# Optimization experiments

Hardware: AMD Instinct MI355X
Metric: run time of the kernel (lower is better)

Reference implementation:

```python
import jax, jax.numpy as jnp
import numpy as np

N = 100000          # num nodes
E_C = 6_400_000     # connection edges
E_D = 400_000       # destination edges
F_IN = 5
H = 8
BN_EPS = 1e-5
L2_EPS = 1e-12


def setup_inputs() -> dict:
    key = jax.random.key(0)
    ks = jax.random.split(key, 16)
    d = {}
    d["x"] = jax.random.normal(ks[0], (N, F_IN), dtype=jnp.float32)
    d["edge_index_connections"] = jax.random.randint(ks[1], (2, E_C), 0, N, dtype=jnp.int64)
    d["edge_index_destinations"] = jax.random.randint(ks[2], (2, E_D), 0, N, dtype=jnp.int64)
    # SAGEConv weights: lin_l (neighbor aggregate), lin_r (root), no bias
    d["W1l"] = jax.random.normal(ks[3], (H, F_IN), jnp.float32) * 0.3
    d["W1r"] = jax.random.normal(ks[4], (H, F_IN), jnp.float32) * 0.3
    d["W2l"] = jax.random.normal(ks[5], (H, H), jnp.float32) * 0.3
    d["W2r"] = jax.random.normal(ks[6], (H, H), jnp.float32) * 0.3
    d["W3l"] = jax.random.normal(ks[7], (H, H), jnp.float32) * 0.3
    d["W3r"] = jax.random.normal(ks[8], (H, H), jnp.float32) * 0.3
    d["W4l"] = jax.random.normal(ks[9], (H, H), jnp.float32) * 0.3
    d["W4r"] = jax.random.normal(ks[10], (H, H), jnp.float32) * 0.3
    # LazyBatchNorm1d affine params (init gamma=1, beta=0)
    for i in range(1, 5):
        d[f"g{i}"] = jnp.ones((H,), jnp.float32)
        d[f"b{i}"] = jnp.zeros((H,), jnp.float32)
    return d


def _sage(x, ei, Wl, Wr):
    # PyG SAGEConv(mean aggr, normalize=True, bias=False):
    # out = lin_l(mean_{j in N(i)} x_j) + lin_r(x_i); then L2 normalize rows.
    src, dst = ei[0], ei[1]
    msgs = x[src]                                            # [E, F] gather
    s = jax.ops.segment_sum(msgs, dst, num_segments=N)       # [N, F]
    cnt = jax.ops.segment_sum(jnp.ones((ei.shape[1],), x.dtype), dst, num_segments=N)
    mean = s / jnp.maximum(cnt, 1.0)[:, None]                # zero for isolated nodes
    out = mean @ Wl.T + x @ Wr.T                             # [N, H]
    nrm = jnp.linalg.norm(out, axis=-1, keepdims=True)
    return out / jnp.maximum(nrm, L2_EPS)


def _bn(x, g, b):
    # BatchNorm1d in training mode: per-feature batch stats (biased variance)
    m = x.mean(axis=0)
    v = x.var(axis=0)
    return (x - m) * jax.lax.rsqrt(v + BN_EPS) * g + b


def reference(x, edge_index_connections, edge_index_destinations,
              W1l, W1r, W2l, W2r, W3l, W3r, W4l, W4r,
              g1, b1, g2, b2, g3, b3, g4, b4):
    eic = edge_index_connections
    eid = edge_index_destinations
    h = _bn(jax.nn.relu(_sage(x, eic, W1l, W1r)), g1, b1)
    # ITERATIONS_BEFORE_DESTINATION = 1 (conv4 + bn2)
    h = _bn(jax.nn.relu(_sage(h, eic, W4l, W4r)), g2, b2)
    # destination pass (conv2 + bn3)
    h = _bn(jax.nn.relu(_sage(h, eid, W2l, W2r)), g3, b3)
    # ITERATIONS_AFTER_DESTINATION = 2 (conv3 + bn4)
    for _ in range(2):
        h = _bn(jax.nn.relu(_sage(h, eic, W3l, W3r)), g4, b4)
    return h
```

## Files before the change

### kernel.cpp

```cpp
#include <hip/hip_runtime.h>
#include <hip/hip_fp16.h>

#define NN 100000
#define EC 6400000
#define ED 400000
#define BN_EPS 1e-5f
#define NB 391
#define CAPC 18432
#define CAPD 2048
#define EPB 8192
#define NBK_C 782
#define NBK_D 49
#define PREPB 16


__global__ __launch_bounds__(1024)
void zero_small(int* __restrict__ cnt_c, int* __restrict__ cnt_d,
                float* __restrict__ stats) {
    int t = threadIdx.x;
    for (int i = t; i < NB; i += 1024) { cnt_c[i] = 0; cnt_d[i] = 0; }
    for (int i = t; i < 5 * 256; i += 1024) stats[i] = 0.f;
}

__global__ __launch_bounds__(1024)
void scatter_fused(const int* __restrict__ eic, const int* __restrict__ eid,
                   int* __restrict__ cnt_c, int* __restrict__ cnt_d,
                   unsigned* __restrict__ packed_c, unsigned* __restrict__ packed_d,
                   const float* __restrict__ x, const float* __restrict__ W1l,
                   const float* __restrict__ W1r, float* __restrict__ xp,
                   __half* __restrict__ xp16,
                   float* __restrict__ W1lp, float* __restrict__ W1rp) {
    int blk = blockIdx.x;
    int tid = threadIdx.x;
    if (blk >= NBK_C + NBK_D) {
        int pb = blk - (NBK_C + NBK_D);
        int t = pb * 1024 + tid;
        if (t < 64) {
            int f = t >> 3, k = t & 7;
            W1lp[t] = (k < 5) ? W1l[f * 5 + k] : 0.f;
            W1rp[t] = (k < 5) ? W1r[f * 5 + k] : 0.f;
        }
        for (int idx = t; idx < NN * 8; idx += PREPB * 1024) {
            int f = idx & 7, i = idx >> 3;
            float v = (f < 5) ? x[i * 5 + f] : 0.f;
            xp[idx] = v;
            xp16[idx] = __float2half(v);
        }
        return;
    }
    const int* ei; int E, cap, base; int* cnt; unsigned* packed;
    if (blk < NBK_C) { ei = eic; E = EC; cnt = cnt_c; packed = packed_c; cap = CAPC; base = blk; }
    else             { ei = eid; E = ED; cnt = cnt_d; packed = packed_d; cap = CAPD; base = blk - NBK_C; }

    __shared__ int h[NB];
    __shared__ int lcur[NB];
    __shared__ int dg[NB];
    __shared__ int ws[16];
    __shared__ int sbuf[EPB];
    __shared__ unsigned short sbkt[EPB];

    for (int i = tid; i < NB; i += 1024) h[i] = 0;
    __syncthreads();
    int beg = base * EPB, end = min(E, beg + EPB);
    int ecnt = end - beg;
    int e0 = beg + tid * 4;
    int e1 = e0 + 4096;
    bool v0 = (e0 < end), v1 = (e1 < end);
    int4 d4a = {0, 0, 0, 0}, d4b = {0, 0, 0, 0};
    if (v0) {
        d4a = *(const int4*)&ei[E + e0];
        atomicAdd(&h[d4a.x >> 8], 1);
        atomicAdd(&h[d4a.y >> 8], 1);
        atomicAdd(&h[d4a.z >> 8], 1);
        atomicAdd(&h[d4a.w >> 8], 1);
    }
    if (v1) {
        d4b = *(const int4*)&ei[E + e1];
        atomicAdd(&h[d4b.x >> 8], 1);
        atomicAdd(&h[d4b.y >> 8], 1);
        atomicAdd(&h[d4b.z >> 8], 1);
        atomicAdd(&h[d4b.w >> 8], 1);
    }
    __syncthreads();
    {
        int v = (tid < NB) ? h[tid] : 0;
        int lane = tid & 63, w = tid >> 6;
        int xx = v;
        #pragma unroll
        for (int sh = 1; sh < 64; sh <<= 1) { int y = __shfl_up(xx, sh); if (lane >= sh) xx += y; }
        if (lane == 63) ws[w] = xx;
        __syncthreads();
        int wb = 0;
        #pragma unroll
        for (int j = 0; j < 16; ++j) if (j < w) wb += ws[j];
        int excl = wb + xx - v;
        if (tid < NB) {
            lcur[tid] = excl;
            int gb = v ? atomicAdd(&cnt[tid], v) : 0;
            dg[tid] = gb - excl;
        }
    }
    __syncthreads();
    if (v0) {
        int4 s4 = *(const int4*)&ei[e0];
        { int b = d4a.x >> 8; int p = atomicAdd(&lcur[b], 1); sbuf[p] = s4.x | ((d4a.x & 255) << 17); sbkt[p] = (unsigned short)b; }
        { int b = d4a.y >> 8; int p = atomicAdd(&lcur[b], 1); sbuf[p] = s4.y | ((d4a.y & 255) << 17); sbkt[p] = (unsigned short)b; }
        { int b = d4a.z >> 8; int p = atomicAdd(&lcur[b], 1); sbuf[p] = s4.z | ((d4a.z & 255) << 17); sbkt[p] = (unsigned short)b; }
        { int b = d4a.w >> 8; int p = atomicAdd(&lcur[b], 1); sbuf[p] = s4.w | ((d4a.w & 255) << 17); sbkt[p] = (unsigned short)b; }
    }
    if (v1) {
        int4 s4 = *(const int4*)&ei[e1];
        { int b = d4b.x >> 8; int p = atomicAdd(&lcur[b], 1); sbuf[p] = s4.x | ((d4b.x & 255) << 17); sbkt[p] = (unsigned short)b; }
        { int b = d4b.y >> 8; int p = atomicAdd(&lcur[b], 1); sbuf[p] = s4.y | ((d4b.y & 255) << 17); sbkt[p] = (unsigned short)b; }
        { int b = d4b.z >> 8; int p = atomicAdd(&lcur[b], 1); sbuf[p] = s4.z | ((d4b.z & 255) << 17); sbkt[p] = (unsigned short)b; }
        { int b = d4b.w >> 8; int p = atomicAdd(&lcur[b], 1); sbuf[p] = s4.w | ((d4b.w & 255) << 17); sbkt[p] = (unsigned short)b; }
    }
    __syncthreads();
    for (int j = tid; j < ecnt; j += 1024) {
        int b = sbkt[j];
        unsigned idx = (unsigned)(dg[b] + j);
        if (idx < (unsigned)cap)
            packed[(size_t)b * cap + idx] = (unsigned)sbuf[j];
    }
}

__global__ __launch_bounds__(1024)
void csr_sort(const unsigned* __restrict__ packed_c, const int* __restrict__ cnt_c,
              int* __restrict__ csr_c, int* __restrict__ offs_c,
              int* __restrict__ deg_c, float* __restrict__ inv_c,
              const unsigned* __restrict__ packed_d, const int* __restrict__ cnt_d,
              int* __restrict__ csr_d, int* __restrict__ offs_d,
              int* __restrict__ deg_d, float* __restrict__ inv_d) {
    __shared__ int h[256];
    __shared__ int loff[256];
    __shared__ int ws[4];
    __shared__ int ebuf[CAPC];
    int blk = blockIdx.x;
    const unsigned* packed; const int* cnt; int cap, b;
    int* csr; int* offs; int* deg; float* inv;
    if (blk < NB) { packed = packed_c; cnt = cnt_c; cap = CAPC; b = blk;
                    csr = csr_c; offs = offs_c; deg = deg_c; inv = inv_c; }
    else          { packed = packed_d; cnt = cnt_d; cap = CAPD; b = blk - NB;
                    csr = csr_d; offs = offs_d; deg = deg_d; inv = inv_d; }
    int tid = threadIdx.x;
    size_t ebeg = (size_t)b * cap;
    int ecnt = min(cnt[b], cap);
    int node0 = b << 8;
    int nn = min(256, NN - node0);
    if (tid < 256) h[tid] = 0;
    __syncthreads();
    for (int e = tid; e < ecnt; e += 1024)
        atomicAdd(&h[packed[ebeg + e] >> 17], 1);
    __syncthreads();
    int v = (tid < 256) ? h[tid] : 0;
    {
        int lane = tid & 63, w = tid >> 6;
        int xx = v;
        #pragma unroll
        for (int sh = 1; sh < 64; sh <<= 1) { int y = __shfl_up(xx, sh); if (lane >= sh) xx += y; }
        if (lane == 63 && w < 4) ws[w] = xx;
        __syncthreads();
        if (tid < 256) {
            int wb = 0;
            #pragma unroll
            for (int j = 0; j < 4; ++j) if (j < w) wb += ws[j];
            int excl = wb + xx - v;
            loff[tid] = excl;
            if (tid < nn) {
                int node = node0 + tid;
                offs[node] = (int)ebeg + excl;
                deg[node]  = v;
                inv[node]  = 1.0f / (float)(v > 1 ? v : 1);
            }
        }
    }
    __syncthreads();
    for (int e = tid; e < ecnt; e += 1024) {
        unsigned u = packed[ebeg + e];
        int p = atomicAdd(&loff[u >> 17], 1);
        ebuf[p] = (int)(u & 0x1FFFF);
    }
    __syncthreads();
    for (int e = tid; e < ecnt; e += 1024) csr[ebeg + e] = ebuf[e];
}

#define ACC8(RV, M) do { \
    float2 q0 = __half22float2(*(const __half2*)&RV.x); \
    float2 q1 = __half22float2(*(const __half2*)&RV.y); \
    float2 q2 = __half22float2(*(const __half2*)&RV.z); \
    float2 q3 = __half22float2(*(const __half2*)&RV.w); \
    a0 = fmaf(q0.x, M, a0); a1 = fmaf(q0.y, M, a1); \
    a2 = fmaf(q1.x, M, a2); a3 = fmaf(q1.y, M, a3); \
    a4 = fmaf(q2.x, M, a4); a5 = fmaf(q2.y, M, a5); \
    a6 = fmaf(q3.x, M, a6); a7 = fmaf(q3.y, M, a7); \
} while (0)

template<bool APPLY_BN>
__global__ __launch_bounds__(256)
void sage_layer8(const float* __restrict__ hin,
                 const __half* __restrict__ hin16,
                 const float* __restrict__ stats_in,
                 const float* __restrict__ gin, const float* __restrict__ bin,
                 const int* __restrict__ offs, const int* __restrict__ deg,
                 const int* __restrict__ csr, const float* __restrict__ inv,
                 const float* __restrict__ Wl, const float* __restrict__ Wr,
                 float* __restrict__ hout, __half* __restrict__ hout16,
                 float* __restrict__ stats_out) {
    __shared__ float bl[16];
    int tid = threadIdx.x;
    if (tid < 16) bl[tid] = 0.f;
    __syncthreads();
    int wave = tid >> 6, lane = tid & 63, g = lane >> 3, f = lane & 7;

    float wls[8], wrs[8];
    float Bl = 0.f, Br = 0.f;
    #pragma unroll
    for (int k = 0; k < 8; ++k) {
        float w_l = Wl[f * 8 + k], w_r = Wr[f * 8 + k];
        float sck = 1.f, shk = 0.f;
        if constexpr (APPLY_BN) {
            float m = stats_in[k * 16] * (1.f / NN);
            float v = stats_in[(8 + k) * 16] * (1.f / NN) - m * m;
            float is = rsqrtf(v + BN_EPS);
            sck = gin[k] * is;
            shk = bin[k] - m * sck;
        }
        wls[k] = sck * w_l;
        wrs[k] = sck * w_r;
        Bl = fmaf(shk, w_l, Bl);
        Br = fmaf(shk, w_r, Br);
    }

    float acc_r = 0.f, acc_r2 = 0.f;
    const int stride = gridDim.x * 32;
    for (int i0 = (blockIdx.x * 4 + wave) * 8; i0 < NN; i0 += stride) {
        int i = i0 + g;
        int ic = min(i, NN - 1);
        bool ok = (i < NN);
        int d = ok ? deg[ic] : 0;
        int o = offs[ic];
        float im = inv[ic];
        const float4* hp = (const float4*)(hin + (size_t)ic * 8);
        float4 h0 = hp[0];
        float4 h1 = hp[1];
        float a0 = 0, a1 = 0, a2 = 0, a3 = 0, a4 = 0, a5 = 0, a6 = 0, a7 = 0;
        for (int b = 0; b < d; b += 32) {
            int e = b + f * 4;
            const int* cp = csr + o + e;
            int c0 = cp[0], c1 = cp[1], c2 = cp[2], c3 = cp[3];
            bool k0 = (e < d), k1 = (e + 1 < d), k2 = (e + 2 < d), k3 = (e + 3 < d);
            unsigned s0 = k0 ? ((unsigned)c0 & 0x1FFFFu) : 0u;
            unsigned s1 = k1 ? ((unsigned)c1 & 0x1FFFFu) : 0u;
            unsigned s2 = k2 ? ((unsigned)c2 & 0x1FFFFu) : 0u;
            unsigned s3 = k3 ? ((unsigned)c3 & 0x1FFFFu) : 0u;
            uint4 r0 = *(const uint4*)(hin16 + (size_t)s0 * 8);
            uint4 r1 = *(const uint4*)(hin16 + (size_t)s1 * 8);
            uint4 r2 = *(const uint4*)(hin16 + (size_t)s2 * 8);
            uint4 r3 = *(const uint4*)(hin16 + (size_t)s3 * 8);
            float m0 = k0 ? 1.f : 0.f;
            float m1 = k1 ? 1.f : 0.f;
            float m2 = k2 ? 1.f : 0.f;
            float m3 = k3 ? 1.f : 0.f;
            ACC8(r0, m0);
            ACC8(r1, m1);
            ACC8(r2, m2);
            ACC8(r3, m3);
        }
        #pragma unroll
        for (int msk = 1; msk < 8; msk <<= 1) {
            a0 += __shfl_xor(a0, msk); a1 += __shfl_xor(a1, msk);
            a2 += __shfl_xor(a2, msk); a3 += __shfl_xor(a3, msk);
            a4 += __shfl_xor(a4, msk); a5 += __shfl_xor(a5, msk);
            a6 += __shfl_xor(a6, msk); a7 += __shfl_xor(a7, msk);
        }
        float dnz = (d > 0) ? 1.f : 0.f;
        float hk[8] = { h0.x, h0.y, h0.z, h0.w, h1.x, h1.y, h1.z, h1.w };
        float ac[8] = { a0, a1, a2, a3, a4, a5, a6, a7 };
        float y = fmaf(dnz, Bl, Br);
        #pragma unroll
        for (int k = 0; k < 8; ++k) {
            y = fmaf(ac[k] * im, wls[k], y);
            y = fmaf(hk[k], wrs[k], y);
        }
        float n2 = y * y;
        n2 += __shfl_xor(n2, 1);
        n2 += __shfl_xor(n2, 2);
        n2 += __shfl_xor(n2, 4);
        float z = y / fmaxf(sqrtf(n2), 1e-12f);
        float r = fmaxf(z, 0.f);
        r = ok ? r : 0.f;
        if (ok) {
            hout[(size_t)i * 8 + f] = r;
            hout16[(size_t)i * 8 + f] = __float2half(r);
        }
        acc_r += r;
        acc_r2 += r * r;
    }
    atomicAdd(&bl[f], acc_r);
    atomicAdd(&bl[8 + f], acc_r2);
    __syncthreads();
    if (tid < 16) atomicAdd(&stats_out[tid * 16], bl[tid]);
}

__global__ void apply_bn_out(const float* __restrict__ hin,
                             const float* __restrict__ stats,
                             const float* __restrict__ g, const float* __restrict__ b,
                             float* __restrict__ out) {
    int t = blockIdx.x * blockDim.x + threadIdx.x;
    if (t >= NN * 8) return;
    int f = t & 7;
    float m = stats[f * 16] * (1.0f / NN);
    float v = stats[(8 + f) * 16] * (1.0f / NN) - m * m;
    float sc = g[f] * rsqrtf(v + BN_EPS);
    float sh = b[f] - m * sc;
    out[t] = fmaf(hin[t], sc, sh);
}


static inline char* bump(char*& p, size_t bytes) {
    char* r = p;
    p += (bytes + 255) & ~(size_t)255;
    return r;
}

extern "C" void kernel_launch(void* const* d_in, const int* in_sizes, int n_in,
                              void* d_out, int out_size, void* d_ws, size_t ws_size,
                              hipStream_t stream) {
    const float* x   = (const float*)d_in[0];
    const int* eic   = (const int*)d_in[1];
    const int* eid   = (const int*)d_in[2];
    const float* W1l = (const float*)d_in[3];
    const float* W1r = (const float*)d_in[4];
    const float* W2l = (const float*)d_in[5];
    const float* W2r = (const float*)d_in[6];
    const float* W3l = (const float*)d_in[7];
    const float* W3r = (const float*)d_in[8];
    const float* W4l = (const float*)d_in[9];
    const float* W4r = (const float*)d_in[10];
    const float* g1 = (const float*)d_in[11];
    const float* b1 = (const float*)d_in[12];
    const float* g2 = (const float*)d_in[13];
    const float* b2 = (const float*)d_in[14];
    const float* g3 = (const float*)d_in[15];
    const float* b3 = (const float*)d_in[16];
    const float* g4 = (const float*)d_in[17];
    const float* b4 = (const float*)d_in[18];
    float* out = (float*)d_out;

    char* p = (char*)d_ws;
    float* stats   = (float*)bump(p, 5 * 256 * 4);
    int*   cnt_c   = (int*)  bump(p, NB * 4);
    int*   cnt_d   = (int*)  bump(p, NB * 4);
    int*   offs_c  = (int*)  bump(p, NN * 4);
    int*   deg_c   = (int*)  bump(p, NN * 4);
    float* inv_c   = (float*)bump(p, NN * 4);
    int*   offs_d  = (int*)  bump(p, NN * 4);
    int*   deg_d   = (int*)  bump(p, NN * 4);
    float* inv_d   = (float*)bump(p, NN * 4);
    int*   csr_c   = (int*)  bump(p, ((size_t)NB * CAPC + 256) * 4);
    int*   csr_d   = (int*)  bump(p, ((size_t)NB * CAPD + 256) * 4);
    float* xp32    = (float*)bump(p, (size_t)NN * 8 * 4);
    __half* xp16   = (__half*)bump(p, (size_t)NN * 8 * 2);
    float* W1lp    = (float*)bump(p, 64 * 4);
    float* W1rp    = (float*)bump(p, 64 * 4);
    unsigned* packed_d = (unsigned*)bump(p, (size_t)NB * CAPD * 4);
    char* pc = p;
    unsigned* packed_c = (unsigned*)bump(p, (size_t)NB * CAPC * 4);
    char* pr = pc;
    float*  r_a   = (float*) bump(pr, (size_t)NN * 8 * 4);
    float*  r_b   = (float*) bump(pr, (size_t)NN * 8 * 4);
    __half* h16_a = (__half*)bump(pr, (size_t)NN * 8 * 2);
    __half* h16_b = (__half*)bump(pr, (size_t)NN * 8 * 2);
    (void)ws_size; (void)in_sizes; (void)n_in; (void)out_size;

    zero_small<<<1, 1024, 0, stream>>>(cnt_c, cnt_d, stats);
    scatter_fused<<<NBK_C + NBK_D + PREPB, 1024, 0, stream>>>(
        eic, eid, cnt_c, cnt_d, packed_c, packed_d,
        x, W1l, W1r, xp32, xp16, W1lp, W1rp);
    csr_sort<<<2 * NB, 1024, 0, stream>>>(
        packed_c, cnt_c, csr_c, offs_c, deg_c, inv_c,
        packed_d, cnt_d, csr_d, offs_d, deg_d, inv_d);

    const int LB = 2048;
    sage_layer8<false><<<LB, 256, 0, stream>>>(
        xp32, xp16, nullptr, nullptr, nullptr,
        offs_c, deg_c, csr_c, inv_c, W1lp, W1rp, r_a, h16_a, stats + 0);
    sage_layer8<true><<<LB, 256, 0, stream>>>(
        r_a, h16_a, stats + 0, g1, b1,
        offs_c, deg_c, csr_c, inv_c, W4l, W4r, r_b, h16_b, stats + 256);
    sage_layer8<true><<<LB, 256, 0, stream>>>(
        r_b, h16_b, stats + 256, g2, b2,
        offs_d, deg_d, csr_d, inv_d, W2l, W2r, r_a, h16_a, stats + 512);
    sage_layer8<true><<<LB, 256, 0, stream>>>(
        r_a, h16_a, stats + 512, g3, b3,
        offs_c, deg_c, csr_c, inv_c, W3l, W3r, r_b, h16_b, stats + 768);
    sage_layer8<true><<<LB, 256, 0, stream>>>(
        r_b, h16_b, stats + 768, g4, b4,
        offs_c, deg_c, csr_c, inv_c, W3l, W3r, r_a, h16_a, stats + 1024);
    apply_bn_out<<<(NN * 8 + 255) / 256, 256, 0, stream>>>(r_a, stats + 1024, g4, b4, out);
}
```

Baseline: 525.9 us.

## Fuse five SAGE layers and final BN into one cooperative kernel

Replaces the six separate layer launches with a single cooperative-groups kernel that runs each SAGE layer and the final BatchNorm apply, using grid-wide syncs between stages. It falls back to the old per-layer launches if the cooperative launch fails. This removes per-launch overhead and idle gaps between kernels. In exchange the grid shrinks to 1024 blocks, which may limit latency hiding in the gather-heavy layers. Grid barriers also add their own cost, and the BN flag becomes a runtime branch instead of a template parameter.

New measurement: 1.071 ms. 104% more time.

```diff
diff --git a/kernel.cpp b/kernel.cpp
--- a/kernel.cpp
+++ b/kernel.cpp
@@ -1,5 +1,7 @@
 #include <hip/hip_runtime.h>
 #include <hip/hip_fp16.h>
+#include <hip/hip_cooperative_groups.h>
+namespace cg = cooperative_groups;
 
 #define NN 100000
 #define EC 6400000
@@ -12,6 +14,7 @@
 #define NBK_C 782
 #define NBK_D 49
 #define PREPB 16
+#define LBC 1024
 
 
 __global__ __launch_bounds__(1024)
@@ -195,18 +198,15 @@
     a6 = fmaf(q3.x, M, a6); a7 = fmaf(q3.y, M, a7); \
 } while (0)
 
-template<bool APPLY_BN>
-__global__ __launch_bounds__(256)
-void sage_layer8(const float* __restrict__ hin,
-                 const __half* __restrict__ hin16,
-                 const float* __restrict__ stats_in,
-                 const float* __restrict__ gin, const float* __restrict__ bin,
-                 const int* __restrict__ offs, const int* __restrict__ deg,
-                 const int* __restrict__ csr, const float* __restrict__ inv,
-                 const float* __restrict__ Wl, const float* __restrict__ Wr,
-                 float* __restrict__ hout, __half* __restrict__ hout16,
-                 float* __restrict__ stats_out) {
-    __shared__ float bl[16];
+__device__ void sage_body(const float* __restrict__ hin,
+                          const __half* __restrict__ hin16,
+                          const float* __restrict__ stats_in,
+                          const float* __restrict__ gin, const float* __restrict__ bin,
+                          const int* __restrict__ offs, const int* __restrict__ deg,
+                          const int* __restrict__ csr, const float* __restrict__ inv,
+                          const float* __restrict__ Wl, const float* __restrict__ Wr,
+                          float* __restrict__ hout, __half* __restrict__ hout16,
+                          float* __restrict__ stats_out, bool apply_bn, float* bl) {
     int tid = threadIdx.x;
     if (tid < 16) bl[tid] = 0.f;
     __syncthreads();
@@ -218,7 +218,7 @@
     for (int k = 0; k < 8; ++k) {
         float w_l = Wl[f * 8 + k], w_r = Wr[f * 8 + k];
         float sck = 1.f, shk = 0.f;
-        if constexpr (APPLY_BN) {
+        if (apply_bn) {
             float m = stats_in[k * 16] * (1.f / NN);
             float v = stats_in[(8 + k) * 16] * (1.f / NN) - m * m;
             float is = rsqrtf(v + BN_EPS);
@@ -302,6 +302,62 @@
     if (tid < 16) atomicAdd(&stats_out[tid * 16], bl[tid]);
 }
 
+__global__ __launch_bounds__(256)
+void mega_sage(const float* xp32, const __half* xp16,
+               float* r_a, __half* h16_a, float* r_b, __half* h16_b,
+               float* stats,
+               const float* g1, const float* b1, const float* g2, const float* b2,
+               const float* g3, const float* b3, const float* g4, const float* b4,
+               const int* offs_c, const int* deg_c, const int* csr_c, const float* inv_c,
+               const int* offs_d, const int* deg_d, const int* csr_d, const float* inv_d,
+               const float* W1lp, const float* W1rp,
+               const float* W2l, const float* W2r,
+               const float* W3l, const float* W3r,
+               const float* W4l, const float* W4r,
+               float* out) {
+    cg::grid_group gg = cg::this_grid();
+    __shared__ float bl[16];
+    sage_body(xp32, xp16, nullptr, nullptr, nullptr,
+              offs_c, deg_c, csr_c, inv_c, W1lp, W1rp, r_a, h16_a, stats + 0, false, bl);
+    gg.sync();
+    sage_body(r_a, h16_a, stats + 0, g1, b1,
+              offs_c, deg_c, csr_c, inv_c, W4l, W4r, r_b, h16_b, stats + 256, true, bl);
+    gg.sync();
+    sage_body(r_b, h16_b, stats + 256, g2, b2,
+              offs_d, deg_d, csr_d, inv_d, W2l, W2r, r_a, h16_a, stats + 512, true, bl);
+    gg.sync();
+    sage_body(r_a, h16_a, stats + 512, g3, b3,
+              offs_c, deg_c, csr_c, inv_c, W3l, W3r, r_b, h16_b, stats + 768, true, bl);
+    gg.sync();
+    sage_body(r_b, h16_b, stats + 768, g4, b4,
+              offs_c, deg_c, csr_c, inv_c, W3l, W3r, r_a, h16_a, stats + 1024, true, bl);
+    gg.sync();
+    const float* st = stats + 1024;
+    for (int t = blockIdx.x * 256 + threadIdx.x; t < NN * 8; t += gridDim.x * 256) {
+        int f = t & 7;
+        float m = st[f * 16] * (1.0f / NN);
+        float v = st[(8 + f) * 16] * (1.0f / NN) - m * m;
+        float sc = g4[f] * rsqrtf(v + BN_EPS);
+        float sh = b4[f] - m * sc;
+        out[t] = fmaf(r_a[t], sc, sh);
+    }
+}
+
+template<bool APPLY_BN>
+__global__ __launch_bounds__(256)
+void sage_layer8(const float* __restrict__ hin, const __half* __restrict__ hin16,
+                 const float* __restrict__ stats_in,
+                 const float* __restrict__ gin, const float* __restrict__ bin,
+                 const int* __restrict__ offs, const int* __restrict__ deg,
+                 const int* __restrict__ csr, const float* __restrict__ inv,
+                 const float* __restrict__ Wl, const float* __restrict__ Wr,
+                 float* __restrict__ hout, __half* __restrict__ hout16,
+                 float* __restrict__ stats_out) {
+    __shared__ float bl[16];
+    sage_body(hin, hin16, stats_in, gin, bin, offs, deg, csr, inv, Wl, Wr,
+              hout, hout16, stats_out, APPLY_BN, bl);
+}
+
 __global__ void apply_bn_out(const float* __restrict__ hin,
                              const float* __restrict__ stats,
                              const float* __restrict__ g, const float* __restrict__ b,
@@ -381,21 +437,39 @@
         packed_c, cnt_c, csr_c, offs_c, deg_c, inv_c,
         packed_d, cnt_d, csr_d, offs_d, deg_d, inv_d);
 
-    const int LB = 2048;
-    sage_layer8<false><<<LB, 256, 0, stream>>>(
-        xp32, xp16, nullptr, nullptr, nullptr,
-        offs_c, deg_c, csr_c, inv_c, W1lp, W1rp, r_a, h16_a, stats + 0);
-    sage_layer8<true><<<LB, 256, 0, stream>>>(
-        r_a, h16_a, stats + 0, g1, b1,
-        offs_c, deg_c, csr_c, inv_c, W4l, W4r, r_b, h16_b, stats + 256);
-    sage_layer8<true><<<LB, 256, 0, stream>>>(
-        r_b, h16_b, stats + 256, g2, b2,
-        offs_d, deg_d, csr_d, inv_d, W2l, W2r, r_a, h16_a, stats + 512);
-    sage_layer8<true><<<LB, 256, 0, stream>>>(
-        r_a, h16_a, stats + 512, g3, b3,
-        offs_c, deg_c, csr_c, inv_c, W3l, W3r, r_b, h16_b, stats + 768);
-    sage_layer8<true><<<LB, 256, 0, stream>>>(
-        r_b, h16_b, stats + 768, g4, b4,
-        offs_c, deg_c, csr_c, inv_c, W3l, W3r, r_a, h16_a, stats + 1024);
-    apply_bn_out<<<(NN * 8 + 255) / 256, 256, 0, stream>>>(r_a, stats + 1024, g4, b4, out);
-}
+    void* margs[] = {
+        (void*)&xp32, (void*)&xp16,
+        (void*)&r_a, (void*)&h16_a, (void*)&r_b, (void*)&h16_b,
+        (void*)&stats,
+        (void*)&g1, (void*)&b1, (void*)&g2, (void*)&b2,
+        (void*)&g3, (void*)&b3, (void*)&g4, (void*)&b4,
+        (void*)&offs_c, (void*)&deg_c, (void*)&csr_c, (void*)&inv_c,
+        (void*)&offs_d, (void*)&deg_d, (void*)&csr_d, (void*)&inv_d,
+        (void*)&W1lp, (void*)&W1rp,
+        (void*)&W2l, (void*)&W2r,
+        (void*)&W3l, (void*)&W3r,
+        (void*)&W4l, (void*)&W4r,
+        (void*)&out
+    };
+    hipError_t ce = hipLaunchCooperativeKernel((void*)mega_sage, dim3(LBC), dim3(256),
+                                               margs, 0, stream);
+    if (ce != hipSuccess) {
+        const int LB = 2048;
+        sage_layer8<false><<<LB, 256, 0, stream>>>(
+            xp32, xp16, nullptr, nullptr, nullptr,
+            offs_c, deg_c, csr_c, inv_c, W1lp, W1rp, r_a, h16_a, stats + 0);
+        sage_layer8<true><<<LB, 256, 0, stream>>>(
+            r_a, h16_a, stats + 0, g1, b1,
+            offs_c, deg_c, csr_c, inv_c, W4l, W4r, r_b, h16_b, stats + 256);
+        sage_layer8<true><<<LB, 256, 0, stream>>>(
+            r_b, h16_b, stats + 256, g2, b2,
+            offs_d, deg_d, csr_d, inv_d, W2l, W2r, r_a, h16_a, stats + 512);
+        sage_layer8<true><<<LB, 256, 0, stream>>>(
+            r_a, h16_a, stats + 512, g3, b3,
+            offs_c, deg_c, csr_c, inv_c, W3l, W3r, r_b, h16_b, stats + 768);
+        sage_layer8<true><<<LB, 256, 0, stream>>>(
+            r_b, h16_b, stats + 768, g4, b4,
+            offs_c, deg_c, csr_c, inv_c, W3l, W3r, r_a, h16_a, stats + 1024);
+        apply_bn_out<<<(NN * 8 + 255) / 256, 256, 0, stream>>>(r_a, stats + 1024, g4, b4, out);
+    }
+}
```
